# Performance work log

Hardware: AMD Instinct MI355X
Metric: run time of the kernel (lower is better)

Reference implementation:

```python
import jax, jax.numpy as jnp
import numpy as np


def setup_inputs() -> dict:
    key = jax.random.key(0)
    k1, k2 = jax.random.split(key)
    B, S, D = 8, 2048, 128
    x = jax.random.normal(k1, (B, S, D), dtype=jnp.float32)
    y = jax.random.normal(k2, (B, S, D), dtype=jnp.float32)
    return {"x": x, "y": y}


def reference(x, y):
    # m1 = x @ y^T  -> [B, Sx, Sy]; unscaled dot-product attention
    m1 = jnp.einsum('bsd,btd->bst', x, y)
    n1 = jax.nn.softmax(m1, axis=-1)
    o1 = jnp.einsum('bst,btd->bsd', n1, y)   # [B, Sx, D]
    a1 = o1 * x                               # gating multiply

    # symmetric pass: m2 = y @ x^T (== m1 transposed)
    m2 = jnp.einsum('btd,bsd->bts', y, x)
    n2 = jax.nn.softmax(m2, axis=-1)
    o2 = jnp.einsum('bts,bsd->btd', n2, x)   # [B, Sy, D]
    a2 = o2 * y

    return jnp.concatenate([a1, a2], axis=-1)  # [B, S, 2D]
```

## Files before the change

kernel.cpp:

```cpp
#include <hip/hip_runtime.h>
#include <hip/hip_bf16.h>

typedef __attribute__((ext_vector_type(8))) short bf16x8;
typedef __attribute__((ext_vector_type(8))) _Float16 f16x8;
typedef __attribute__((ext_vector_type(4))) float f32x4;
typedef __attribute__((ext_vector_type(16))) float f32x16;

#define MFMA16B(a, b, c) __builtin_amdgcn_mfma_f32_16x16x32_bf16(a, b, c, 0, 0, 0)
#define MFMA32F(a, b, c) __builtin_amdgcn_mfma_f32_32x32x16_f16(a, b, c, 0, 0, 0)

static constexpr int S = 2048;
static constexpr int D = 128;

__device__ inline unsigned short f2b(float f) {
    union { float f; unsigned int u; } v; v.f = f;
    unsigned int u = v.u;
    return (unsigned short)((u + 0x7FFFu + ((u >> 16) & 1u)) >> 16);
}
__device__ inline float b2f(unsigned short h) {
    union { unsigned int u; float f; } v; v.u = ((unsigned int)h) << 16;
    return v.f;
}
__device__ inline unsigned int pack2(float a, float b) {
    return (unsigned int)f2b(a) | ((unsigned int)f2b(b) << 16);
}
__device__ inline unsigned int pkh(float a, float b) {
    union { _Float16 h; unsigned short u; } ua, ub;
    ua.h = (_Float16)a; ub.h = (_Float16)b;
    return (unsigned int)ua.u | ((unsigned int)ub.u << 16);
}

__device__ __forceinline__ void gload16(const void* g, void* l) {
    __builtin_amdgcn_global_load_lds(
        (const __attribute__((address_space(1))) unsigned int*)(unsigned long long)(g),
        (__attribute__((address_space(3))) unsigned int*)(unsigned int)(unsigned long long)(l),
        16, 0, 0);
}

__global__ __launch_bounds__(256) void bimodal_prep5(
    const float* __restrict__ X, const float* __restrict__ Y,
    unsigned short* __restrict__ WS)
{
    const int bid = blockIdx.x;
    const int t = bid & 63;
    const int b = (bid >> 6) & 7;
    const int mat = bid >> 9;
    const float* src = mat ? Y : X;
    char* kf = (char*)(WS + (size_t)(mat * 2 + 0) * (8ull * S * D)) + (size_t)(b * 64 + t) * 8192;
    char* vt = (char*)(WS + (size_t)(mat * 2 + 1) * (8ull * S * D)) + (size_t)(b * 64 + t) * 8192;

    __shared__ float ftile[32][129];
    const int tid = threadIdx.x;
    const float* tsrc = src + ((size_t)(b * S + t * 32)) * D;
#pragma unroll
    for (int it = 0; it < 4; ++it) {
        int idx = tid + it * 256;
        int row = idx >> 5, ch = idx & 31;
        float4 v = *(const float4*)(tsrc + (size_t)row * D + ch * 4);
        ftile[row][ch * 4 + 0] = v.x; ftile[row][ch * 4 + 1] = v.y;
        ftile[row][ch * 4 + 2] = v.z; ftile[row][ch * 4 + 3] = v.w;
    }
    __syncthreads();
#pragma unroll
    for (int it = 0; it < 8; ++it) {
        int w = tid + it * 256;
        int row = w >> 6, cp = w & 63;
        unsigned int d = pkh(ftile[row][2 * cp], ftile[row][2 * cp + 1]);
        int byte = (row * 256 + cp * 4) ^ ((row & 7) << 4);
        *(unsigned int*)(kf + byte) = d;
    }
#pragma unroll
    for (int it = 0; it < 8; ++it) {
        int w = tid + it * 256;
        int dd = w >> 4, jp = w & 15;
        unsigned int d = pkh(ftile[2 * jp][dd], ftile[2 * jp + 1][dd]);
        int byte = (dd * 64 + jp * 4) ^ ((dd & 7) << 4);
        *(unsigned int*)(vt + byte) = d;
    }
}

__global__ __launch_bounds__(512) void bimodal_attn_v5(
    const float* __restrict__ X, const float* __restrict__ Y,
    const unsigned short* __restrict__ WS, float* __restrict__ Out)
{
    const int orig = blockIdx.x;
    const int wg = (orig & 7) * 32 + (orig >> 3);
    const int qt = wg & 15;
    const int p  = (wg >> 4) & 1;
    const int b  = wg >> 5;

    const float* Q = p ? Y : X;
    const int kvmat = p ? 0 : 1;
    const int ocol = p * D;

    __shared__ __align__(16) char smem[65536];

    const int tid = threadIdx.x;
    const int wv = tid >> 6;
    const int lane = tid & 63;
    const int qp = lane & 31;
    const int h = lane >> 5;
    const int grp = wv >> 2;
    const int qb = wv & 3;
    const int i0 = qt * 128 + qb * 32;

    const float* qrow = Q + ((size_t)(b * S + i0 + qp)) * D;
    f16x8 qf[8];
#pragma unroll
    for (int kc = 0; kc < 8; ++kc) {
        const float* qpp = qrow + kc * 16 + h * 8;
        float4 f0 = *(const float4*)qpp;
        float4 f1 = *(const float4*)(qpp + 4);
        f16x8 tq;
        tq[0] = (_Float16)f0.x; tq[1] = (_Float16)f0.y; tq[2] = (_Float16)f0.z; tq[3] = (_Float16)f0.w;
        tq[4] = (_Float16)f1.x; tq[5] = (_Float16)f1.y; tq[6] = (_Float16)f1.z; tq[7] = (_Float16)f1.w;
        qf[kc] = tq;
    }

    f32x16 o[4];
#pragma unroll
    for (int db = 0; db < 4; ++db)
#pragma unroll
        for (int i = 0; i < 16; ++i) o[db][i] = 0.f;
    float m = -1e30f, l = 0.f;

    const char* kfb = (const char*)(WS + (size_t)(kvmat * 2 + 0) * (8ull * S * D)) + (size_t)b * (S * D * 2);
    const char* vtb = (const char*)(WS + (size_t)(kvmat * 2 + 1) * (8ull * S * D)) + (size_t)b * (S * D * 2);
    const int gl = qb * 64 + lane;
    char* mybase = smem + grp * 32768;

    auto stage = [&](int t, int bi) {
        char* kb = mybase + bi * 16384;
        char* vb = kb + 8192;
        const char* kt = kfb + t * 8192;
        const char* vp = vtb + t * 8192;
        gload16(kt + gl * 16, kb + gl * 16);
        gload16(kt + 4096 + gl * 16, kb + 4096 + gl * 16);
        gload16(vp + gl * 16, vb + gl * 16);
        gload16(vp + 4096 + gl * 16, vb + 4096 + gl * 16);
    };

    stage(grp, 0);
    __syncthreads();

    for (int s = 0; s < 32; ++s) {
        if (s < 31) stage(2 * (s + 1) + grp, (s + 1) & 1);
        const char* kb = mybase + (s & 1) * 16384;
        const char* vb = kb + 8192;

        f32x16 sT;
#pragma unroll
        for (int i = 0; i < 16; ++i) sT[i] = 0.f;
        __builtin_amdgcn_s_setprio(1);
#pragma unroll
        for (int kc = 0; kc < 8; ++kc) {
            int byte = (qp * 256 + kc * 32 + h * 16) ^ ((qp & 7) << 4);
            f16x8 kA = *(const f16x8*)(kb + byte);
            sT = MFMA32F(kA, qf[kc], sT);
        }
        __builtin_amdgcn_s_setprio(0);

        float pmax = sT[0];
#pragma unroll
        for (int i = 1; i < 16; ++i) pmax = fmaxf(pmax, sT[i]);
        pmax = fmaxf(pmax, __shfl_xor(pmax, 32));
        if (!__all(pmax - m <= 8.f)) {
            float mn = fmaxf(m, pmax);
            float alpha = __expf(m - mn);
            m = mn; l *= alpha;
#pragma unroll
            for (int db = 0; db < 4; ++db)
#pragma unroll
                for (int i = 0; i < 16; ++i) o[db][i] *= alpha;
        }
        float rs = 0.f;
#pragma unroll
        for (int i = 0; i < 16; ++i) { sT[i] = __expf(sT[i] - m); rs += sT[i]; }
        rs += __shfl_xor(rs, 32);
        l += rs;

        unsigned w8[8];
#pragma unroll
        for (int t2 = 0; t2 < 4; ++t2) {
            w8[2 * t2]     = pkh(sT[4 * t2 + 0], sT[4 * t2 + 1]);
            w8[2 * t2 + 1] = pkh(sT[4 * t2 + 2], sT[4 * t2 + 3]);
        }
        union { unsigned u[4]; f16x8 v; } bf0, bf1;
#pragma unroll
        for (int v2 = 0; v2 < 2; ++v2) {
            unsigned a0 = w8[v2], b0 = w8[2 + v2];
            asm volatile("v_permlane32_swap_b32 %0, %1" : "+v"(a0), "+v"(b0));
            bf0.u[v2] = a0; bf0.u[2 + v2] = b0;
            unsigned a1 = w8[4 + v2], b1 = w8[6 + v2];
            asm volatile("v_permlane32_swap_b32 %0, %1" : "+v"(a1), "+v"(b1));
            bf1.u[v2] = a1; bf1.u[2 + v2] = b1;
        }

        __builtin_amdgcn_s_setprio(1);
#pragma unroll
        for (int db = 0; db < 4; ++db) {
            int rowbyte = (db * 32 + qp) * 64;
            int x0 = (rowbyte + h * 16) ^ ((qp & 7) << 4);
            int x1 = (rowbyte + 32 + h * 16) ^ ((qp & 7) << 4);
            f16x8 v0 = *(const f16x8*)(vb + x0);
            f16x8 v1 = *(const f16x8*)(vb + x1);
            o[db] = MFMA32F(v0, bf0.v, o[db]);
            o[db] = MFMA32F(v1, bf1.v, o[db]);
        }
        __builtin_amdgcn_s_setprio(0);

        __syncthreads();
    }

    {
        float2* mlp = (float2*)(smem + wv * 512);
        mlp[lane] = make_float2(m, l);
    }
    __syncthreads();
    float2 pml = ((float2*)(smem + (wv ^ 4) * 512))[lane];
    float mstar = fmaxf(m, pml.x);
    float sc = __expf(m - mstar);
    float lstar = sc * l + __expf(pml.x - mstar) * pml.y;
#pragma unroll
    for (int db = 0; db < 4; ++db)
#pragma unroll
        for (int i = 0; i < 16; ++i) o[db][i] *= sc;
    __syncthreads();

    float* obuf = (float*)(smem + 4096) + qb * 1024 + lane * 16;
#pragma unroll
    for (int db = 0; db < 4; ++db) {
        if (grp == 1) {
#pragma unroll
            for (int i = 0; i < 16; ++i) obuf[i] = o[db][i];
        }
        __syncthreads();
        if (grp == 0) {
#pragma unroll
            for (int i = 0; i < 16; ++i) o[db][i] += obuf[i];
        }
        __syncthreads();
    }

    if (grp == 0) {
        const float invl = 1.f / lstar;
        float* outr = Out + ((size_t)(b * S + i0 + qp)) * (2 * D) + ocol;
#pragma unroll
        for (int db = 0; db < 4; ++db)
#pragma unroll
            for (int t2 = 0; t2 < 4; ++t2) {
                int d0 = db * 32 + t2 * 8 + h * 4;
                float4 qv = *(const float4*)(qrow + d0);
                float4 ov;
                ov.x = o[db][4 * t2 + 0] * invl * qv.x;
                ov.y = o[db][4 * t2 + 1] * invl * qv.y;
                ov.z = o[db][4 * t2 + 2] * invl * qv.z;
                ov.w = o[db][4 * t2 + 3] * invl * qv.w;
                *(float4*)(outr + d0) = ov;
            }
    }
}

__global__ __launch_bounds__(256) void bimodal_attn_fb(
    const float* __restrict__ X, const float* __restrict__ Y,
    float* __restrict__ Out)
{
    const int bid = blockIdx.x;
    const int qt = bid & 31;
    const int p  = (bid >> 5) & 1;
    const int b  = bid >> 6;

    const float* Q  = p ? Y : X;
    const float* KV = p ? X : Y;
    const int ocol = p * D;

    __shared__ unsigned short Khi[64 * D];
    __shared__ unsigned short Klo[64 * D];
    __shared__ unsigned short Vt[D * 64];
    __shared__ unsigned short Psh[4][16 * 72];

    const int tid = threadIdx.x;
    const int wv = tid >> 6;
    const int lane = tid & 63;
    const int c = lane & 15;
    const int g = lane >> 4;
    const int i0 = qt * 64 + wv * 16;

    const float* qbase = Q + ((size_t)(b * S + i0 + c)) * D;
    bf16x8 qhi[4], qlo[4];
#pragma unroll
    for (int kc = 0; kc < 4; ++kc) {
        const float* qp = qbase + kc * 32 + g * 8;
        float4 f0 = *(const float4*)qp;
        float4 f1 = *(const float4*)(qp + 4);
        float fv[8] = {f0.x, f0.y, f0.z, f0.w, f1.x, f1.y, f1.z, f1.w};
        bf16x8 th, tl;
#pragma unroll
        for (int i = 0; i < 8; ++i) {
            unsigned short hh = f2b(fv[i]);
            th[i] = (short)hh;
            tl[i] = (short)f2b(fv[i] - b2f(hh));
        }
        qhi[kc] = th; qlo[kc] = tl;
    }

    f32x4 o[8];
#pragma unroll
    for (int nb = 0; nb < 8; ++nb) { o[nb][0] = 0.f; o[nb][1] = 0.f; o[nb][2] = 0.f; o[nb][3] = 0.f; }
    float m[4], l[4];
#pragma unroll
    for (int r = 0; r < 4; ++r) { m[r] = -1e30f; l[r] = 0.f; }

    const float* kvb = KV + (size_t)b * S * D;
    unsigned short* pbuf = Psh[wv];

    for (int j0 = 0; j0 < S; j0 += 64) {
#pragma unroll
        for (int t = 0; t < 4; ++t) {
            int task = tid + t * 256;
            int jr = task >> 4, sl = task & 15;
            const float* src = kvb + (size_t)(j0 + jr) * D + sl * 8;
            float4 f0 = *(const float4*)src;
            float4 f1 = *(const float4*)(src + 4);
            float fv[8] = {f0.x, f0.y, f0.z, f0.w, f1.x, f1.y, f1.z, f1.w};
            unsigned short hv[8];
            float lv[8];
#pragma unroll
            for (int i = 0; i < 8; ++i) {
                hv[i] = f2b(fv[i]);
                lv[i] = fv[i] - b2f(hv[i]);
            }
            uint4 wh, wl;
            wh.x = (unsigned int)hv[0] | ((unsigned int)hv[1] << 16);
            wh.y = (unsigned int)hv[2] | ((unsigned int)hv[3] << 16);
            wh.z = (unsigned int)hv[4] | ((unsigned int)hv[5] << 16);
            wh.w = (unsigned int)hv[6] | ((unsigned int)hv[7] << 16);
            wl.x = pack2(lv[0], lv[1]); wl.y = pack2(lv[2], lv[3]);
            wl.z = pack2(lv[4], lv[5]); wl.w = pack2(lv[6], lv[7]);
            int byte = (jr * 256 + sl * 16) ^ ((jr & 7) << 4);
            *(uint4*)((char*)Khi + byte) = wh;
            *(uint4*)((char*)Klo + byte) = wl;
        }
#pragma unroll
        for (int t = 0; t < 2; ++t) {
            int task = tid + t * 256;
            int jp = task & 31, dc = task >> 5;
            const float* s0 = kvb + (size_t)(j0 + 2 * jp) * D + dc * 8;
            const float* s1 = s0 + D;
            float4 a0 = *(const float4*)s0, a1 = *(const float4*)(s0 + 4);
            float4 b0 = *(const float4*)s1, b1 = *(const float4*)(s1 + 4);
            float av[8] = {a0.x, a0.y, a0.z, a0.w, a1.x, a1.y, a1.z, a1.w};
            float bv[8] = {b0.x, b0.y, b0.z, b0.w, b1.x, b1.y, b1.z, b1.w};
#pragma unroll
            for (int i = 0; i < 8; ++i) {
                int d = dc * 8 + i;
                int byte = (d * 128 + jp * 4) ^ ((d & 7) << 4);
                *(unsigned int*)((char*)Vt + byte) = pack2(av[i], bv[i]);
            }
        }
        __syncthreads();

        f32x4 sF[4];
#pragma unroll
        for (int nb = 0; nb < 4; ++nb) {
            f32x4 acc; acc[0] = 0.f; acc[1] = 0.f; acc[2] = 0.f; acc[3] = 0.f;
#pragma unroll
            for (int kc = 0; kc < 4; ++kc) {
                int row = nb * 16 + c;
                int byte = (row * 256 + (kc * 32 + g * 8) * 2) ^ ((row & 7) << 4);
                bf16x8 kh = *(const bf16x8*)((char*)Khi + byte);
                bf16x8 kl = *(const bf16x8*)((char*)Klo + byte);
                acc = MFMA16B(qhi[kc], kh, acc);
                acc = MFMA16B(qhi[kc], kl, acc);
                acc = MFMA16B(qlo[kc], kh, acc);
            }
            sF[nb] = acc;
        }

#pragma unroll
        for (int r = 0; r < 4; ++r) {
            float v = fmaxf(fmaxf(sF[0][r], sF[1][r]), fmaxf(sF[2][r], sF[3][r]));
            v = fmaxf(v, __shfl_xor(v, 1));
            v = fmaxf(v, __shfl_xor(v, 2));
            v = fmaxf(v, __shfl_xor(v, 4));
            v = fmaxf(v, __shfl_xor(v, 8));
            float mn = fmaxf(m[r], v);
            float alpha = __expf(m[r] - mn);
            m[r] = mn;
            float rs = 0.f;
#pragma unroll
            for (int nb = 0; nb < 4; ++nb) {
                float pv = __expf(sF[nb][r] - mn);
                sF[nb][r] = pv;
                rs += pv;
            }
            rs += __shfl_xor(rs, 1);
            rs += __shfl_xor(rs, 2);
            rs += __shfl_xor(rs, 4);
            rs += __shfl_xor(rs, 8);
            l[r] = l[r] * alpha + rs;
#pragma unroll
            for (int nb = 0; nb < 8; ++nb) o[nb][r] *= alpha;
        }

#pragma unroll
        for (int nb = 0; nb < 4; ++nb)
#pragma unroll
            for (int r = 0; r < 4; ++r)
                pbuf[(g * 4 + r) * 72 + nb * 16 + c] = f2b(sF[nb][r]);

        bf16x8 pa[2];
#pragma unroll
        for (int kc = 0; kc < 2; ++kc)
            pa[kc] = *(const bf16x8*)(pbuf + c * 72 + kc * 32 + g * 8);

#pragma unroll
        for (int nb = 0; nb < 8; ++nb) {
#pragma unroll
            for (int kc = 0; kc < 2; ++kc) {
                int d = nb * 16 + c;
                int byte = (d * 128 + (kc * 32 + g * 8) * 2) ^ ((d & 7) << 4);
                bf16x8 vf = *(const bf16x8*)((char*)Vt + byte);
                o[nb] = MFMA16B(pa[kc], vf, o[nb]);
            }
        }
        __syncthreads();
    }

    float* outb = Out + ((size_t)(b * S + i0)) * (2 * D) + ocol;
    const float* qg = Q + (size_t)(b * S + i0) * D;
#pragma unroll
    for (int r = 0; r < 4; ++r) {
        int row = g * 4 + r;
        float inv = 1.f / l[r];
#pragma unroll
        for (int nb = 0; nb < 8; ++nb) {
            int col = nb * 16 + c;
            float qv = qg[(size_t)row * D + col];
            outb[(size_t)row * (2 * D) + col] = o[nb][r] * inv * qv;
        }
    }
}

extern "C" void kernel_launch(void* const* d_in, const int* in_sizes, int n_in,
                              void* d_out, int out_size, void* d_ws, size_t ws_size,
                              hipStream_t stream) {
    const float* x = (const float*)d_in[0];
    const float* y = (const float*)d_in[1];
    float* out = (float*)d_out;
    const size_t need = 4ull * 8 * S * D * 2;
    if (ws_size >= need) {
        hipLaunchKernelGGL(bimodal_prep5, dim3(1024), dim3(256), 0, stream,
                           x, y, (unsigned short*)d_ws);
        hipLaunchKernelGGL(bimodal_attn_v5, dim3(256), dim3(512), 0, stream,
                           x, y, (const unsigned short*)d_ws, out);
    } else {
        hipLaunchKernelGGL(bimodal_attn_fb, dim3(512), dim3(256), 0, stream, x, y, out);
    }
}
```

Measured before the change: 66.18 us.

## Process two KV tiles per stage with larger LDS double buffers

Each stage now loads two 64-key K/V tiles per wave group into a doubled 128 KB LDS buffer, which halves the number of barriers and loop iterations. The two QK^T MFMA chains are issued back to back before the softmax and PV steps. Each wave group now takes a contiguous half of the KV sequence instead of interleaved tiles. The cross-group reduction buffer layout is also changed so lanes write with a stride of 64 to avoid LDS bank conflicts. Using 128 KB of LDS per block limits occupancy to one block per CU and adds register pressure from the two live score tiles.

```diff
diff --git a/kernel.cpp b/kernel.cpp
--- a/kernel.cpp
+++ b/kernel.cpp
@@ -79,7 +79,7 @@
     }
 }
 
-__global__ __launch_bounds__(512) void bimodal_attn_v5(
+__global__ __launch_bounds__(512) void bimodal_attn_v7(
     const float* __restrict__ X, const float* __restrict__ Y,
     const unsigned short* __restrict__ WS, float* __restrict__ Out)
 {
@@ -93,7 +93,7 @@
     const int kvmat = p ? 0 : 1;
     const int ocol = p * D;
 
-    __shared__ __align__(16) char smem[65536];
+    __shared__ __align__(16) char smem[131072];
 
     const int tid = threadIdx.x;
     const int wv = tid >> 6;
@@ -127,39 +127,34 @@
     const char* kfb = (const char*)(WS + (size_t)(kvmat * 2 + 0) * (8ull * S * D)) + (size_t)b * (S * D * 2);
     const char* vtb = (const char*)(WS + (size_t)(kvmat * 2 + 1) * (8ull * S * D)) + (size_t)b * (S * D * 2);
     const int gl = qb * 64 + lane;
-    char* mybase = smem + grp * 32768;
-
-    auto stage = [&](int t, int bi) {
-        char* kb = mybase + bi * 16384;
-        char* vb = kb + 8192;
-        const char* kt = kfb + t * 8192;
-        const char* vp = vtb + t * 8192;
-        gload16(kt + gl * 16, kb + gl * 16);
-        gload16(kt + 4096 + gl * 16, kb + 4096 + gl * 16);
-        gload16(vp + gl * 16, vb + gl * 16);
-        gload16(vp + 4096 + gl * 16, vb + 4096 + gl * 16);
+    char* mybase = smem + grp * 65536;
+
+    auto stage = [&](int ps, int bi) {
+        char* kb = mybase + bi * 32768;
+        const char* kt = kfb + (size_t)(32 * grp + 2 * ps) * 8192;
+        const char* vp = vtb + (size_t)(32 * grp + 2 * ps) * 8192;
+#pragma unroll
+        for (int i = 0; i < 4; ++i)
+            gload16(kt + gl * 16 + i * 4096, kb + gl * 16 + i * 4096);
+#pragma unroll
+        for (int i = 0; i < 4; ++i)
+            gload16(vp + gl * 16 + i * 4096, kb + 16384 + gl * 16 + i * 4096);
     };
 
-    stage(grp, 0);
-    __syncthreads();
-
-    for (int s = 0; s < 32; ++s) {
-        if (s < 31) stage(2 * (s + 1) + grp, (s + 1) & 1);
-        const char* kb = mybase + (s & 1) * 16384;
-        const char* vb = kb + 8192;
-
+    auto qkt = [&](const char* kb) {
         f32x16 sT;
 #pragma unroll
         for (int i = 0; i < 16; ++i) sT[i] = 0.f;
-        __builtin_amdgcn_s_setprio(1);
 #pragma unroll
         for (int kc = 0; kc < 8; ++kc) {
             int byte = (qp * 256 + kc * 32 + h * 16) ^ ((qp & 7) << 4);
             f16x8 kA = *(const f16x8*)(kb + byte);
             sT = MFMA32F(kA, qf[kc], sT);
         }
-        __builtin_amdgcn_s_setprio(0);
-
+        return sT;
+    };
+
+    auto smpv = [&](f32x16& sT, const char* vb) {
         float pmax = sT[0];
 #pragma unroll
         for (int i = 1; i < 16; ++i) pmax = fmaxf(pmax, sT[i]);
@@ -208,6 +203,22 @@
             o[db] = MFMA32F(v1, bf1.v, o[db]);
         }
         __builtin_amdgcn_s_setprio(0);
+    };
+
+    stage(0, 0);
+    __syncthreads();
+
+    for (int s = 0; s < 16; ++s) {
+        if (s < 15) stage(s + 1, (s + 1) & 1);
+        const char* kb = mybase + (s & 1) * 32768;
+
+        __builtin_amdgcn_s_setprio(1);
+        f32x16 s0 = qkt(kb);
+        f32x16 s1 = qkt(kb + 8192);
+        __builtin_amdgcn_s_setprio(0);
+
+        smpv(s0, kb + 16384);
+        smpv(s1, kb + 24576);
 
         __syncthreads();
     }
@@ -227,17 +238,17 @@
         for (int i = 0; i < 16; ++i) o[db][i] *= sc;
     __syncthreads();
 
-    float* obuf = (float*)(smem + 4096) + qb * 1024 + lane * 16;
+    float* ob = (float*)(smem + 4096);
 #pragma unroll
     for (int db = 0; db < 4; ++db) {
         if (grp == 1) {
 #pragma unroll
-            for (int i = 0; i < 16; ++i) obuf[i] = o[db][i];
+            for (int i = 0; i < 16; ++i) ob[qb * 1024 + i * 64 + lane] = o[db][i];
         }
         __syncthreads();
         if (grp == 0) {
 #pragma unroll
-            for (int i = 0; i < 16; ++i) o[db][i] += obuf[i];
+            for (int i = 0; i < 16; ++i) o[db][i] += ob[qb * 1024 + i * 64 + lane];
         }
         __syncthreads();
     }
@@ -452,7 +463,7 @@
     if (ws_size >= need) {
         hipLaunchKernelGGL(bimodal_prep5, dim3(1024), dim3(256), 0, stream,
                            x, y, (unsigned short*)d_ws);
-        hipLaunchKernelGGL(bimodal_attn_v5, dim3(256), dim3(512), 0, stream,
+        hipLaunchKernelGGL(bimodal_attn_v7, dim3(256), dim3(512), 0, stream,
                            x, y, (const unsigned short*)d_ws, out);
     } else {
         hipLaunchKernelGGL(bimodal_attn_fb, dim3(512), dim3(256), 0, stream, x, y, out);
```

After: 64.22 us, median of 4. 3.0% less time.
